# Optimization experiments

Hardware: AMD Instinct MI355X
Metric: run time of the kernel (lower is better)

## Reference

```python
import jax, jax.numpy as jnp
import numpy as np

B, NQ, NV, DIM, HEADS, K = 2, 2048, 2048, 256, 8, 8
HD = DIM // HEADS
HID = 4 * DIM
SCALE = HD ** -0.5
EPS = 1e-5


def setup_inputs() -> dict:
    key = jax.random.key(0)
    ks = jax.random.split(key, 40)
    r = lambda i, s: jax.random.normal(ks[i], s, jnp.float32) * 0.02
    inp = {
        'q': jax.random.normal(ks[0], (B, NQ, DIM), jnp.float32),
        'v': jax.random.normal(ks[1], (B, NV, DIM), jnp.float32),
        'q_pos': jax.random.normal(ks[2], (B, NQ, 3), jnp.float32),
        'v_pos': jax.random.normal(ks[3], (B, NV, 3), jnp.float32),
        'self_knn_index': jax.random.randint(ks[4], (B, NQ, K), 0, NQ, jnp.int32),
        'cross_knn_index': jax.random.randint(ks[5], (B, NQ, K), 0, NV, jnp.int32),
        # LayerNorms (gamma=1, beta=0)
        'norm1_g': jnp.ones(DIM), 'norm1_b': jnp.zeros(DIM),
        'normq_g': jnp.ones(DIM), 'normq_b': jnp.zeros(DIM),
        'normv_g': jnp.ones(DIM), 'normv_b': jnp.zeros(DIM),
        'norm2_g': jnp.ones(DIM), 'norm2_b': jnp.zeros(DIM),
        # self-attention (qkv_bias=False), proj has bias
        'sa_qkv_w': r(6, (DIM, 3 * DIM)),
        'sa_proj_w': r(7, (DIM, DIM)), 'sa_proj_b': jnp.zeros(DIM),
        # cross-attention: q proj and kv proj (no bias), out proj with bias
        'ca_q_w': r(8, (DIM, DIM)),
        'ca_kv_w': r(9, (DIM, 2 * DIM)),
        'ca_proj_w': r(10, (DIM, DIM)), 'ca_proj_b': jnp.zeros(DIM),
        # MLP
        'fc1_w': r(11, (DIM, HID)), 'fc1_b': jnp.zeros(HID),
        'fc2_w': r(12, (HID, DIM)), 'fc2_b': jnp.zeros(DIM),
        # kNN maps
        'knn_w': r(13, (2 * DIM, DIM)), 'knn_b': jnp.zeros(DIM),
        'merge_w': r(14, (2 * DIM, DIM)), 'merge_b': jnp.zeros(DIM),
        'knnx_w': r(15, (2 * DIM, DIM)), 'knnx_b': jnp.zeros(DIM),
        'mergex_w': r(16, (2 * DIM, DIM)), 'mergex_b': jnp.zeros(DIM),
    }
    return inp


def _ln(x, g, b):
    m = x.mean(-1, keepdims=True)
    var = x.var(-1, keepdims=True)
    return (x - m) / jnp.sqrt(var + EPS) * g + b


def _heads(x):  # [B,N,DIM] -> [B,H,N,HD]
    Bx, N, _ = x.shape
    return x.reshape(Bx, N, HEADS, HD).transpose(0, 2, 1, 3)


def _attend(qh, kh, vh, proj_w, proj_b):
    a = jax.nn.softmax(jnp.einsum('bhqd,bhkd->bhqk', qh, kh) * SCALE, axis=-1)
    o = jnp.einsum('bhqk,bhkd->bhqd', a, vh)
    Bx, _, N, _ = o.shape
    o = o.transpose(0, 2, 1, 3).reshape(Bx, N, DIM)
    return o @ proj_w + proj_b


_gather = jax.vmap(lambda pts, idx: pts[idx])  # ([N,D],[Nq,K]) -> [Nq,K,D]


def _knn_feature(qn, vn, idx):  # gather -> diff/cat -> [B,Nq,K,2D]
    local = _gather(vn, idx)                      # [B,Nq,K,D]
    qe = qn[:, :, None, :]                        # [B,Nq,1,D]
    return jnp.concatenate([local - qe, jnp.broadcast_to(qe, local.shape)], -1)


def reference(q, v, q_pos, v_pos, self_knn_index, cross_knn_index,
              norm1_g, norm1_b, normq_g, normq_b, normv_g, normv_b,
              norm2_g, norm2_b, sa_qkv_w, sa_proj_w, sa_proj_b,
              ca_q_w, ca_kv_w, ca_proj_w, ca_proj_b,
              fc1_w, fc1_b, fc2_w, fc2_b,
              knn_w, knn_b, merge_w, merge_b,
              knnx_w, knnx_b, mergex_w, mergex_b):
    # ---- self-attention block with self-kNN branch ----
    nq = _ln(q, norm1_g, norm1_b)
    qkv = nq @ sa_qkv_w
    qh, kh, vh = (_heads(t) for t in jnp.split(qkv, 3, axis=-1))
    sa_out = _attend(qh, kh, vh, sa_proj_w, sa_proj_b)
    f = _knn_feature(nq, nq, self_knn_index)
    knn_out = jax.nn.leaky_relu(f @ knn_w + knn_b, 0.2).max(axis=-2)
    q1 = jnp.concatenate([sa_out, knn_out], -1) @ merge_w + merge_b
    q = q + q1
    # ---- cross-attention block with cross-kNN branch ----
    nq2 = _ln(q, normq_g, normq_b)
    nv = _ln(v, normv_g, normv_b)
    qh = _heads(nq2 @ ca_q_w)
    kh, vh = (_heads(t) for t in jnp.split(nv @ ca_kv_w, 2, axis=-1))
    ca_out = _attend(qh, kh, vh, ca_proj_w, ca_proj_b)
    f = _knn_feature(nq2, nv, cross_knn_index)
    knnx_out = jax.nn.leaky_relu(f @ knnx_w + knnx_b, 0.2).max(axis=-2)
    q2 = jnp.concatenate([ca_out, knnx_out], -1) @ mergex_w + mergex_b
    q = q + q2
    # ---- MLP block ----
    h = _ln(q, norm2_g, norm2_b)
    h = jax.nn.gelu(h @ fc1_w + fc1_b, approximate=False)
    q = q + (h @ fc2_w + fc2_b)
    return q
```

## Files before the change

kernel.cpp:

```cpp
#include <hip/hip_runtime.h>
#include <math.h>

#define NQC   2048
#define NKVC  2048
#define DIMC  256
#define SCALEF 0.2550348810731232f

typedef short bfrag __attribute__((ext_vector_type(8)));
typedef float ffrag __attribute__((ext_vector_type(4)));
typedef unsigned short us8 __attribute__((ext_vector_type(8)));

__device__ __forceinline__ float gelu_exact(float x) {
    return 0.5f * x * (1.0f + erff(x * 0.70710678118654752f));
}
__device__ __forceinline__ unsigned short f2bf(float f) {
    union { float f; unsigned u; } v; v.f = f;
    unsigned r = v.u + 0x7FFFu + ((v.u >> 16) & 1u);
    return (unsigned short)(r >> 16);
}
__device__ __forceinline__ float bf2f(unsigned short u) {
    union { unsigned u; float f; } v; v.u = ((unsigned)u) << 16;
    return v.f;
}
__device__ __forceinline__ float fexp2(float x) {
    float r; asm("v_exp_f32 %0, %1" : "=v"(r) : "v"(x)); return r;
}
__device__ __forceinline__ unsigned cvt_pk_bf16(float lo, float hi) {
    unsigned r; asm("v_cvt_pk_bf16_f32 %0, %1, %2" : "=v"(r) : "v"(lo), "v"(hi));
    return r;
}

__device__ __forceinline__ void ln_row(
    const float* __restrict__ x, const float* __restrict__ g,
    const float* __restrict__ b, unsigned short* __restrict__ y, int row)
{
    int lane = threadIdx.x & 63;
    const float* xr = x + (size_t)row * DIMC + lane * 4;
    float4 vv = *(const float4*)xr;
    float s  = vv.x + vv.y + vv.z + vv.w;
    float sq = vv.x*vv.x + vv.y*vv.y + vv.z*vv.z + vv.w*vv.w;
    #pragma unroll
    for (int off = 32; off >= 1; off >>= 1) {
        s  += __shfl_xor(s, off);
        sq += __shfl_xor(sq, off);
    }
    float mean = s * (1.0f/DIMC);
    float inv  = rsqrtf(sq * (1.0f/DIMC) - mean*mean + 1e-5f);
    float4 gg = *(const float4*)(g + lane*4);
    float4 bb = *(const float4*)(b + lane*4);
    ushort4 o;
    o.x = f2bf((vv.x - mean) * inv * gg.x + bb.x);
    o.y = f2bf((vv.y - mean) * inv * gg.y + bb.y);
    o.z = f2bf((vv.z - mean) * inv * gg.z + bb.z);
    o.w = f2bf((vv.w - mean) * inv * gg.w + bb.w);
    *(ushort4*)(y + (size_t)row * DIMC + lane * 4) = o;
}

__global__ __launch_bounds__(256) void prep_ln(
    const float* __restrict__ qkv, const float* __restrict__ knn,
    const float* __restrict__ proj, const float* __restrict__ merge,
    const float* __restrict__ caq, const float* __restrict__ knnx,
    const float* __restrict__ cakv, const float* __restrict__ projx,
    const float* __restrict__ mergex, const float* __restrict__ fc1,
    const float* __restrict__ fc2, unsigned short* __restrict__ dst,
    const float* __restrict__ lx, const float* __restrict__ lg,
    const float* __restrict__ lb, unsigned short* __restrict__ ly,
    const float* __restrict__ vx, const float* __restrict__ vg,
    const float* __restrict__ vb, unsigned short* __restrict__ vy,
    const float* __restrict__ pb1, const float* __restrict__ mb1, float* __restrict__ bf1o,
    const float* __restrict__ pbx, const float* __restrict__ mbx, float* __restrict__ bfxo)
{
    if (blockIdx.x >= 3584) {
        const float* bp = (blockIdx.x == 3584) ? pb1 : pbx;
        const float* Wm = (blockIdx.x == 3584) ? merge : mergex;
        const float* bm = (blockIdx.x == 3584) ? mb1 : mbx;
        float* o        = (blockIdx.x == 3584) ? bf1o : bfxo;
        int m = threadIdx.x;
        float acc = bm[m];
        for (int k = 0; k < 256; ++k) acc += bp[k] * Wm[(size_t)k * 256 + m];
        o[m] = acc;
        return;
    }
    if (blockIdx.x >= 2560) {
        int row = (blockIdx.x - 2560) * 4 + (threadIdx.x >> 6);
        ln_row(vx, vg, vb, vy, row);
        return;
    }
    if (blockIdx.x >= 1536) {
        int row = (blockIdx.x - 1536) * 4 + (threadIdx.x >> 6);
        ln_row(lx, lg, lb, ly, row);
        return;
    }
    int e = (blockIdx.x * 256 + threadIdx.x) * 4;
    float v[4];
    float scale = 1.0f;
    if (e < 327680) {
        int n = e >> 8, k = e & 255;
        if (n < 768) {
            const float* s = qkv + (size_t)k * 768 + n;
            #pragma unroll
            for (int i = 0; i < 4; ++i) v[i] = s[(size_t)i * 768];
            if (n < 256) scale = SCALEF;
        } else if (n < 1024) {
            const float* s = knn + (size_t)k * 256 + (n - 768);
            #pragma unroll
            for (int i = 0; i < 4; ++i) v[i] = s[(size_t)i * 256];
        } else {
            const float* s = knn + (size_t)k * 256 + (n - 1024);
            #pragma unroll
            for (int i = 0; i < 4; ++i) v[i] = s[65536 + (size_t)i * 256] - s[(size_t)i * 256];
        }
    } else if (e < 393216) {
        int l = e - 327680;
        const float* s = proj + l;
        #pragma unroll
        for (int i = 0; i < 4; ++i) v[i] = s[i];
    } else if (e < 524288) {
        int l = e - 393216, n = l >> 9, k = l & 511;
        const float* s = merge + (size_t)k * 256 + n;
        #pragma unroll
        for (int i = 0; i < 4; ++i) v[i] = s[(size_t)i * 256];
    } else if (e < 655360) {
        int l = e - 524288, n = l >> 8, k = l & 255;
        if (n < 256) {
            const float* s = caq + (size_t)k * 256 + n;
            #pragma unroll
            for (int i = 0; i < 4; ++i) v[i] = s[(size_t)i * 256];
            scale = SCALEF;
        } else {
            const float* s = knnx + (size_t)k * 256 + (n - 256);
            #pragma unroll
            for (int i = 0; i < 4; ++i) v[i] = s[65536 + (size_t)i * 256] - s[(size_t)i * 256];
        }
    } else if (e < 851968) {
        int l = e - 655360, n = l >> 8, k = l & 255;
        if (n < 512) {
            const float* s = cakv + (size_t)k * 512 + n;
            #pragma unroll
            for (int i = 0; i < 4; ++i) v[i] = s[(size_t)i * 512];
        } else {
            const float* s = knnx + (size_t)k * 256 + (n - 512);
            #pragma unroll
            for (int i = 0; i < 4; ++i) v[i] = s[(size_t)i * 256];
        }
    } else if (e < 917504) {
        int l = e - 851968;
        const float* s = projx + l;
        #pragma unroll
        for (int i = 0; i < 4; ++i) v[i] = s[i];
    } else if (e < 1048576) {
        int l = e - 917504, n = l >> 9, k = l & 511;
        const float* s = mergex + (size_t)k * 256 + n;
        #pragma unroll
        for (int i = 0; i < 4; ++i) v[i] = s[(size_t)i * 256];
    } else if (e < 1310720) {
        int l = e - 1048576, n = l >> 8, k = l & 255;
        const float* s = fc1 + (size_t)k * 1024 + n;
        #pragma unroll
        for (int i = 0; i < 4; ++i) v[i] = s[(size_t)i * 1024];
    } else {
        int l = e - 1310720, n = l >> 10, k = l & 1023;
        const float* s = fc2 + (size_t)k * 256 + n;
        #pragma unroll
        for (int i = 0; i < 4; ++i) v[i] = s[(size_t)i * 256];
    }
    ushort4 o;
    o.x = f2bf(v[0] * scale); o.y = f2bf(v[1] * scale);
    o.z = f2bf(v[2] * scale); o.w = f2bf(v[3] * scale);
    *(ushort4*)(dst + e) = o;
}

__global__ __launch_bounds__(256) void ln_b(
    const float* __restrict__ x, const float* __restrict__ g,
    const float* __restrict__ b, unsigned short* __restrict__ y)
{
    ln_row(x, g, b, y, blockIdx.x * 4 + (threadIdx.x >> 6));
}

template<int ACT, int RESID, int OUTBF>
__device__ __forceinline__ void gemm_body(
    const unsigned short* __restrict__ A, int lda,
    const unsigned short* __restrict__ Wt,
    const float* __restrict__ bias,
    const float* __restrict__ resid, int ldr,
    void* __restrict__ Cp, int ldc, int Kc, int row0, int col0,
    unsigned short (* __restrict__ Alds)[72],
    unsigned short (* __restrict__ Wlds)[72])
{
    const int tid = threadIdx.x;
    const int wid = tid >> 6, lane = tid & 63;
    const int lm = lane & 15, quad = lane >> 4;
    const int wr = wid >> 1, wc = wid & 1;
    const int ar = tid >> 2, ac = (tid & 3) * 16;
    const unsigned short* Ag = A  + (size_t)(row0 + ar) * lda + ac;
    const unsigned short* Wg = Wt + (size_t)(col0 + ar) * Kc  + ac;

    us8 a0 = *(const us8*)Ag;
    us8 a1 = *(const us8*)(Ag + 8);
    us8 w0 = *(const us8*)Wg;
    us8 w1 = *(const us8*)(Wg + 8);

    ffrag acc[2][2];
    #pragma unroll
    for (int mi = 0; mi < 2; ++mi)
        #pragma unroll
        for (int ni = 0; ni < 2; ++ni)
            acc[mi][ni] = (ffrag){0.f, 0.f, 0.f, 0.f};

    for (int k0 = 0;;) {
        __syncthreads();
        *(us8*)&Alds[ar][ac]   = a0;
        *(us8*)&Alds[ar][ac+8] = a1;
        *(us8*)&Wlds[ar][ac]   = w0;
        *(us8*)&Wlds[ar][ac+8] = w1;
        __syncthreads();
        k0 += 64;
        if (k0 < Kc) {
            a0 = *(const us8*)(Ag + k0);
            a1 = *(const us8*)(Ag + k0 + 8);
            w0 = *(const us8*)(Wg + k0);
            w1 = *(const us8*)(Wg + k0 + 8);
        }
        #pragma unroll
        for (int kc = 0; kc < 2; ++kc) {
            bfrag af[2], bw[2];
            #pragma unroll
            for (int mi = 0; mi < 2; ++mi)
                af[mi] = *(const bfrag*)&Alds[wr*32 + mi*16 + lm][kc*32 + quad*8];
            #pragma unroll
            for (int ni = 0; ni < 2; ++ni)
                bw[ni] = *(const bfrag*)&Wlds[wc*32 + ni*16 + lm][kc*32 + quad*8];
            #pragma unroll
            for (int mi = 0; mi < 2; ++mi)
                #pragma unroll
                for (int ni = 0; ni < 2; ++ni)
                    acc[mi][ni] = __builtin_amdgcn_mfma_f32_16x16x32_bf16(
                        af[mi], bw[ni], acc[mi][ni], 0, 0, 0);
        }
        if (k0 >= Kc) break;
    }
    #pragma unroll
    for (int mi = 0; mi < 2; ++mi) {
        #pragma unroll
        for (int ni = 0; ni < 2; ++ni) {
            int gr = row0 + wr*32 + mi*16 + quad*4;
            int gc = col0 + wc*32 + ni*16 + lm;
            float bv = bias ? bias[gc] : 0.f;
            #pragma unroll
            for (int r = 0; r < 4; ++r) {
                float o = acc[mi][ni][r] + bv;
                if (ACT == 1) o = gelu_exact(o);
                if (RESID) o += resid[(size_t)(gr + r) * ldr + gc];
                if (OUTBF) ((unsigned short*)Cp)[(size_t)(gr + r) * ldc + gc] = f2bf(o);
                else       ((float*)Cp)[(size_t)(gr + r) * ldc + gc] = o;
            }
        }
    }
}

template<int ACT, int RESID, int OUTBF>
__global__ __launch_bounds__(256) void gemm64(
    const unsigned short* __restrict__ A, int lda,
    const unsigned short* __restrict__ Wt,
    const float* __restrict__ bias,
    const float* __restrict__ resid, int ldr,
    void* __restrict__ Cp, int ldc, int Kc)
{
    __shared__ unsigned short Alds[64][72];
    __shared__ unsigned short Wlds[64][72];
    gemm_body<ACT,RESID,OUTBF>(A, lda, Wt, bias, resid, ldr, Cp, ldc, Kc,
                               blockIdx.y * 64, blockIdx.x * 64, Alds, Wlds);
}

__global__ __launch_bounds__(256) void gemm_qkv_fold(
    const unsigned short* __restrict__ XB, const unsigned short* __restrict__ WT1,
    unsigned short* __restrict__ A1,
    const unsigned short* __restrict__ WTmerge, const unsigned short* __restrict__ projbf,
    unsigned short* __restrict__ WTf1,
    const unsigned short* __restrict__ WTmergex, const unsigned short* __restrict__ projxbf,
    unsigned short* __restrict__ WTfx)
{
    __shared__ unsigned short Alds[64][72];
    __shared__ unsigned short Wlds[64][72];
    const unsigned short *A, *Wt; unsigned short* C;
    int lda, ldc, row0, col0;
    if (blockIdx.y >= 64) {
        if (blockIdx.x >= 16) return;
        row0 = (blockIdx.x >> 2) * 64; col0 = (blockIdx.x & 3) * 64;
        lda = 512; ldc = 256;
        if (blockIdx.y == 64) { A = WTmerge;  Wt = projbf;  C = WTf1; }
        else                  { A = WTmergex; Wt = projxbf; C = WTfx; }
    } else {
        A = XB; Wt = WT1; C = A1; lda = 256; ldc = 1280;
        row0 = blockIdx.y * 64; col0 = blockIdx.x * 64;
    }
    gemm_body<0,0,1>(A, lda, Wt, nullptr, nullptr, 0, C, ldc, 256, row0, col0, Alds, Wlds);
}

template<int ACT, int RESID, int OUTBF>
__global__ __launch_bounds__(512) void gemm64x8(
    const unsigned short* __restrict__ A, int lda,
    const unsigned short* __restrict__ Wt,
    const float* __restrict__ bias,
    const float* __restrict__ resid, int ldr,
    void* __restrict__ Cp, int ldc, int Kc)
{
    __shared__ unsigned short Alds[2][64][72];
    __shared__ unsigned short Wlds[2][64][72];
    __shared__ float Red[64][68];
    const int tid = threadIdx.x;
    const int g = tid >> 8;
    const int t = tid & 255;
    const int wid2 = (tid >> 6) & 3, lane = tid & 63;
    const int lm = lane & 15, quad = lane >> 4;
    const int wr = wid2 >> 1, wc = wid2 & 1;
    const int row0 = blockIdx.y * 64, col0 = blockIdx.x * 64;
    const int ar = t >> 2, ac = (t & 3) * 16;
    const int KH = Kc >> 1;
    const unsigned short* Ag = A  + (size_t)(row0 + ar) * lda + g * KH + ac;
    const unsigned short* Wg = Wt + (size_t)(col0 + ar) * Kc  + g * KH + ac;

    us8 a0 = *(const us8*)Ag;
    us8 a1 = *(const us8*)(Ag + 8);
    us8 w0 = *(const us8*)Wg;
    us8 w1 = *(const us8*)(Wg + 8);

    ffrag acc[2][2];
    #pragma unroll
    for (int mi = 0; mi < 2; ++mi)
        #pragma unroll
        for (int ni = 0; ni < 2; ++ni)
            acc[mi][ni] = (ffrag){0.f, 0.f, 0.f, 0.f};

    for (int k0 = 0;;) {
        __syncthreads();
        *(us8*)&Alds[g][ar][ac]   = a0;
        *(us8*)&Alds[g][ar][ac+8] = a1;
        *(us8*)&Wlds[g][ar][ac]   = w0;
        *(us8*)&Wlds[g][ar][ac+8] = w1;
        __syncthreads();
        k0 += 64;
        if (k0 < KH) {
            a0 = *(const us8*)(Ag + k0);
            a1 = *(const us8*)(Ag + k0 + 8);
            w0 = *(const us8*)(Wg + k0);
            w1 = *(const us8*)(Wg + k0 + 8);
        }
        #pragma unroll
        for (int kc = 0; kc < 2; ++kc) {
            bfrag af[2], bw[2];
            #pragma unroll
            for (int mi = 0; mi < 2; ++mi)
                af[mi] = *(const bfrag*)&Alds[g][wr*32 + mi*16 + lm][kc*32 + quad*8];
            #pragma unroll
            for (int ni = 0; ni < 2; ++ni)
                bw[ni] = *(const bfrag*)&Wlds[g][wc*32 + ni*16 + lm][kc*32 + quad*8];
            #pragma unroll
            for (int mi = 0; mi < 2; ++mi)
                #pragma unroll
                for (int ni = 0; ni < 2; ++ni)
                    acc[mi][ni] = __builtin_amdgcn_mfma_f32_16x16x32_bf16(
                        af[mi], bw[ni], acc[mi][ni], 0, 0, 0);
        }
        if (k0 >= KH) break;
    }
    __syncthreads();
    if (g == 1) {
        #pragma unroll
        for (int mi = 0; mi < 2; ++mi)
            #pragma unroll
            for (int ni = 0; ni < 2; ++ni) {
                int lr = wr*32 + mi*16 + quad*4;
                int lc = wc*32 + ni*16 + lm;
                #pragma unroll
                for (int r = 0; r < 4; ++r)
                    Red[lr + r][lc] = acc[mi][ni][r];
            }
    }
    __syncthreads();
    if (g == 0) {
        #pragma unroll
        for (int mi = 0; mi < 2; ++mi) {
            #pragma unroll
            for (int ni = 0; ni < 2; ++ni) {
                int lr = wr*32 + mi*16 + quad*4;
                int lc = wc*32 + ni*16 + lm;
                int gr = row0 + lr;
                int gc = col0 + lc;
                float bv = bias ? bias[gc] : 0.f;
                #pragma unroll
                for (int r = 0; r < 4; ++r) {
                    float o = acc[mi][ni][r] + Red[lr + r][lc] + bv;
                    if (ACT == 1) o = gelu_exact(o);
                    if (RESID) o += resid[(size_t)(gr + r) * ldr + gc];
                    if (OUTBF) ((unsigned short*)Cp)[(size_t)(gr + r) * ldc + gc] = f2bf(o);
                    else       ((float*)Cp)[(size_t)(gr + r) * ldc + gc] = o;
                }
            }
        }
    }
}

__global__ __launch_bounds__(512) void gemm64x8f(
    const unsigned short* __restrict__ Op, const float* __restrict__ Lp,
    const unsigned short* __restrict__ Akn,
    const unsigned short* __restrict__ Wat,
    const unsigned short* __restrict__ Wkn,
    const float* __restrict__ bias,
    const float* __restrict__ resid,
    float* __restrict__ Cp)
{
    __shared__ unsigned short Alds[2][64][72];
    __shared__ unsigned short Wlds[2][64][72];
    __shared__ float Red[64][68];
    const int tid = threadIdx.x;
    const int g = tid >> 8;
    const int t = tid & 255;
    const int wid2 = (tid >> 6) & 3, lane = tid & 63;
    const int lm = lane & 15, quad = lane >> 4;
    const int wr = wid2 >> 1, wc = wid2 & 1;
    const int row0 = blockIdx.y * 64, col0 = blockIdx.x * 64;
    const int ar = t >> 2, ac = (t & 3) * 16;
    const int grow = row0 + ar;

    const unsigned short* O0 = Op + (size_t)grow * 256 + ac;
    const unsigned short* O1 = Op + (size_t)(4096 + grow) * 256 + ac;
    const float* L0 = Lp + (size_t)grow * 8;
    const float* L1 = Lp + (size_t)(4096 + grow) * 8;
    const unsigned short* Ak = Akn + (size_t)grow * 512 + ac;
    const unsigned short* Wg = g ? Wkn + (size_t)(col0 + ar) * 512 + ac
                                 : Wat + (size_t)(col0 + ar) * 256 + ac;

    us8 a0, a1, o10, o11;
    float li = 0.f;
    if (g == 0) {
        a0  = *(const us8*)O0;  a1  = *(const us8*)(O0 + 8);
        o10 = *(const us8*)O1;  o11 = *(const us8*)(O1 + 8);
        li  = 1.0f / (L0[ac >> 5] + L1[ac >> 5]);
    } else {
        a0 = *(const us8*)Ak;   a1 = *(const us8*)(Ak + 8);
    }
    us8 w0 = *(const us8*)Wg;
    us8 w1 = *(const us8*)(Wg + 8);

    ffrag acc[2][2];
    #pragma unroll
    for (int mi = 0; mi < 2; ++mi)
        #pragma unroll
        for (int ni = 0; ni < 2; ++ni)
            acc[mi][ni] = (ffrag){0.f, 0.f, 0.f, 0.f};

    for (int k0 = 0;;) {
        us8 s0 = a0, s1 = a1;
        if (g == 0) {
            #pragma unroll
            for (int i = 0; i < 8; ++i) {
                s0[i] = f2bf((bf2f(a0[i]) + bf2f(o10[i])) * li);
                s1[i] = f2bf((bf2f(a1[i]) + bf2f(o11[i])) * li);
            }
        }
        __syncthreads();
        *(us8*)&Alds[g][ar][ac]   = s0;
        *(us8*)&Alds[g][ar][ac+8] = s1;
        *(us8*)&Wlds[g][ar][ac]   = w0;
        *(us8*)&Wlds[g][ar][ac+8] = w1;
        __syncthreads();
        k0 += 64;
        if (k0 < 256) {
            if (g == 0) {
                a0  = *(const us8*)(O0 + k0);  a1  = *(const us8*)(O0 + k0 + 8);
                o10 = *(const us8*)(O1 + k0);  o11 = *(const us8*)(O1 + k0 + 8);
                li  = 1.0f / (L0[(k0 + ac) >> 5] + L1[(k0 + ac) >> 5]);
            } else {
                a0 = *(const us8*)(Ak + k0);   a1 = *(const us8*)(Ak + k0 + 8);
            }
            w0 = *(const us8*)(Wg + k0);
            w1 = *(const us8*)(Wg + k0 + 8);
        }
        #pragma unroll
        for (int kc = 0; kc < 2; ++kc) {
            bfrag af[2], bw[2];
            #pragma unroll
            for (int mi = 0; mi < 2; ++mi)
                af[mi] = *(const bfrag*)&Alds[g][wr*32 + mi*16 + lm][kc*32 + quad*8];
            #pragma unroll
            for (int ni = 0; ni < 2; ++ni)
                bw[ni] = *(const bfrag*)&Wlds[g][wc*32 + ni*16 + lm][kc*32 + quad*8];
            #pragma unroll
            for (int mi = 0; mi < 2; ++mi)
                #pragma unroll
                for (int ni = 0; ni < 2; ++ni)
                    acc[mi][ni] = __builtin_amdgcn_mfma_f32_16x16x32_bf16(
                        af[mi], bw[ni], acc[mi][ni], 0, 0, 0);
        }
        if (k0 >= 256) break;
    }
    __syncthreads();
    if (g == 1) {
        #pragma unroll
        for (int mi = 0; mi < 2; ++mi)
            #pragma unroll
            for (int ni = 0; ni < 2; ++ni) {
                int lr = wr*32 + mi*16 + quad*4;
                int lc = wc*32 + ni*16 + lm;
                #pragma unroll
                for (int r = 0; r < 4; ++r)
                    Red[lr + r][lc] = acc[mi][ni][r];
            }
    }
    __syncthreads();
    if (g == 0) {
        #pragma unroll
        for (int mi = 0; mi < 2; ++mi) {
            #pragma unroll
            for (int ni = 0; ni < 2; ++ni) {
                int lr = wr*32 + mi*16 + quad*4;
                int lc = wc*32 + ni*16 + lm;
                int gr = row0 + lr;
                int gc = col0 + lc;
                float bv = bias[gc];
                #pragma unroll
                for (int r = 0; r < 4; ++r)
                    Cp[(size_t)(gr + r) * 256 + gc] =
                        acc[mi][ni][r] + Red[lr + r][lc] + bv
                        + resid[(size_t)(gr + r) * 256 + gc];
            }
        }
    }
}

__global__ __launch_bounds__(256) void gemm64_dual(
    const unsigned short* __restrict__ XB,
    const unsigned short* __restrict__ NVB,
    const unsigned short* __restrict__ WT2,
    const unsigned short* __restrict__ WT3,
    unsigned short* __restrict__ A2,
    unsigned short* __restrict__ A3)
{
    __shared__ unsigned short Alds[64][72];
    __shared__ unsigned short Wlds[64][72];
    const unsigned short* A; const unsigned short* Wt;
    unsigned short* C; int ldc, col0;
    if (blockIdx.x < 8) { A = XB;  Wt = WT2; C = A2; ldc = 512; col0 = blockIdx.x * 64; }
    else                { A = NVB; Wt = WT3; C = A3; ldc = 768; col0 = (blockIdx.x - 8) * 64; }
    gemm_body<0,0,1>(A, 256, Wt, nullptr, nullptr, 0, C, ldc, 256,
                     blockIdx.y * 64, col0, Alds, Wlds);
}

__global__ __launch_bounds__(256) void attn_gather(
    const unsigned short* __restrict__ Qp, int ldq,
    const unsigned short* __restrict__ Kp, int ldk,
    const unsigned short* __restrict__ Vp, int ldv,
    unsigned short* __restrict__ Op, float* __restrict__ Lp,
    const unsigned short* __restrict__ P, int ldp,
    const unsigned short* __restrict__ Base, int ldb,
    const float* __restrict__ gbias, const int* __restrict__ idx,
    unsigned short* __restrict__ gout, int ldgo)
{
    __shared__ unsigned short Klds[64][40];
    __shared__ __align__(16) unsigned short Vt[32][72];
    __shared__ __align__(16) unsigned short Plds[4][16][72];
    int tid = threadIdx.x, wid = tid >> 6, lane = tid & 63;

    if (blockIdx.z >= 4) {
        int gbid = blockIdx.x + 32 * (blockIdx.y + 8 * (blockIdx.z - 4));
        int q = gbid * 4 + wid;
        int b = q >> 11;
        int c = lane * 4;
        ushort4 bu = *(const ushort4*)(Base + (size_t)q * ldb + c);
        float4 bi = *(const float4*)(gbias + c);
        float bsx = bf2f(bu.x) + bi.x, bsy = bf2f(bu.y) + bi.y;
        float bsz = bf2f(bu.z) + bi.z, bsw = bf2f(bu.w) + bi.w;
        float4 acc = make_float4(-3e38f, -3e38f, -3e38f, -3e38f);
        const int* ip = idx + (size_t)q * 8;
        #pragma unroll
        for (int k = 0; k < 8; ++k) {
            int j = ip[k];
            ushort4 pu = *(const ushort4*)(P + ((size_t)(b * NKVC + j)) * ldp + c);
            float t;
            t = bsx + bf2f(pu.x); t = t > 0.f ? t : 0.2f * t; acc.x = fmaxf(acc.x, t);
            t = bsy + bf2f(pu.y); t = t > 0.f ? t : 0.2f * t; acc.y = fmaxf(acc.y, t);
            t = bsz + bf2f(pu.z); t = t > 0.f ? t : 0.2f * t; acc.z = fmaxf(acc.z, t);
            t = bsw + bf2f(pu.w); t = t > 0.f ? t : 0.2f * t; acc.w = fmaxf(acc.w, t);
        }
        ushort4 o;
        o.x = f2bf(acc.x); o.y = f2bf(acc.y); o.z = f2bf(acc.z); o.w = f2bf(acc.w);
        *(ushort4*)(gout + (size_t)q * ldgo + c) = o;
        return;
    }

    int zc = blockIdx.z, bb = zc >> 1, ck = zc & 1;
    int h = blockIdx.y;
    int hoff = h * 32;
    int lm = lane & 15, quad = lane >> 4;
    size_t qbase  = (size_t)bb * NQC;
    size_t kvbase = (size_t)bb * NKVC;
    int q0 = blockIdx.x * 64 + wid * 16;

    bfrag aq = *(const bfrag*)(Qp + (qbase + q0 + lm) * (size_t)ldq + hoff + quad * 8);

    float l_r[4] = {0.f, 0.f, 0.f, 0.f};
    ffrag oacc[2];
    oacc[0] = (ffrag){0.f, 0.f, 0.f, 0.f};
    oacc[1] = (ffrag){0.f, 0.f, 0.f, 0.f};

    const int kkey = tid >> 2, kd0 = (tid & 3) * 8;
    const int vkey = tid & 63, vd0 = (tid >> 6) * 8;
    const int vcol = ((vkey & 15) << 2) | (vkey >> 4);
    const unsigned short* kg0 = Kp + (kvbase + kkey) * (size_t)ldk + hoff + kd0;
    const unsigned short* vg0 = Vp + (kvbase + vkey) * (size_t)ldv + hoff + vd0;

    for (int kt = ck * 16; kt < ck * 16 + 16; ++kt) {
        us8 kv = *(const us8*)(kg0 + (size_t)kt * 64 * ldk);
        us8 vv = *(const us8*)(vg0 + (size_t)kt * 64 * ldv);
        __syncthreads();
        *(us8*)&Klds[kkey][kd0] = kv;
        #pragma unroll
        for (int i = 0; i < 8; ++i) Vt[vd0 + i][vcol] = vv[i];
        __syncthreads();

        ffrag sacc[4];
        #pragma unroll
        for (int t = 0; t < 4; ++t) {
            bfrag bk = *(const bfrag*)&Klds[t*16 + lm][quad * 8];
            sacc[t] = __builtin_amdgcn_mfma_f32_16x16x32_bf16(
                aq, bk, (ffrag){0.f,0.f,0.f,0.f}, 0, 0, 0);
        }

        #pragma unroll
        for (int r = 0; r < 4; ++r) {
            float p0 = fexp2(sacc[0][r]), p1 = fexp2(sacc[1][r]);
            float p2 = fexp2(sacc[2][r]), p3 = fexp2(sacc[3][r]);
            l_r[r] += (p0 + p1) + (p2 + p3);
            unsigned u0 = cvt_pk_bf16(p0, p1);
            unsigned u1 = cvt_pk_bf16(p2, p3);
            *(uint2*)&Plds[wid][quad*4 + r][lm << 2] = make_uint2(u0, u1);
        }
        asm volatile("s_waitcnt lgkmcnt(0)" ::: "memory");

        #pragma unroll
        for (int kc = 0; kc < 2; ++kc) {
            bfrag ap = *(const bfrag*)&Plds[wid][lm][kc*32 + quad*8];
            #pragma unroll
            for (int nt = 0; nt < 2; ++nt) {
                bfrag bv = *(const bfrag*)&Vt[nt*16 + lm][kc*32 + quad*8];
                oacc[nt] = __builtin_amdgcn_mfma_f32_16x16x32_bf16(
                    ap, bv, oacc[nt], 0, 0, 0);
            }
        }
    }
    #pragma unroll
    for (int nt = 0; nt < 2; ++nt)
        #pragma unroll
        for (int r = 0; r < 4; ++r)
            Op[((size_t)ck * 4096 + qbase + q0 + quad*4 + r) * 256 + hoff + nt*16 + lm]
                = f2bf(oacc[nt][r]);
    #pragma unroll
    for (int r = 0; r < 4; ++r) {
        float l = l_r[r];
        l += __shfl_xor(l, 1);
        l += __shfl_xor(l, 2);
        l += __shfl_xor(l, 4);
        l += __shfl_xor(l, 8);
        if (lm == 0)
            Lp[((size_t)ck * 4096 + qbase + q0 + quad*4 + r) * 8 + h] = l;
    }
}

extern "C" void kernel_launch(void* const* d_in, const int* in_sizes, int n_in,
                              void* d_out, int out_size, void* d_ws, size_t ws_size,
                              hipStream_t stream) {
    const float* q_in   = (const float*)d_in[0];
    const float* v_in   = (const float*)d_in[1];
    const int*   idx_s  = (const int*)d_in[4];
    const int*   idx_x  = (const int*)d_in[5];
    const float* n1g = (const float*)d_in[6],  *n1b = (const float*)d_in[7];
    const float* nqg = (const float*)d_in[8],  *nqb = (const float*)d_in[9];
    const float* nvg = (const float*)d_in[10], *nvb = (const float*)d_in[11];
    const float* n2g = (const float*)d_in[12], *n2b = (const float*)d_in[13];
    const float* sa_qkv_w  = (const float*)d_in[14];
    const float* sa_proj_w = (const float*)d_in[15];
    const float* sa_proj_b = (const float*)d_in[16];
    const float* ca_q_w    = (const float*)d_in[17];
    const float* ca_kv_w   = (const float*)d_in[18];
    const float* ca_proj_w = (const float*)d_in[19];
    const float* ca_proj_b = (const float*)d_in[20];
    const float* fc1_w = (const float*)d_in[21], *fc1_b = (const float*)d_in[22];
    const float* fc2_w = (const float*)d_in[23], *fc2_b = (const float*)d_in[24];
    const float* knn_w   = (const float*)d_in[25], *knn_b   = (const float*)d_in[26];
    const float* merge_w = (const float*)d_in[27], *merge_b = (const float*)d_in[28];
    const float* knnx_w  = (const float*)d_in[29], *knnx_b  = (const float*)d_in[30];
    const float* mergex_w = (const float*)d_in[31], *mergex_b = (const float*)d_in[32];
    float* out = (float*)d_out;

    unsigned short* A1      = (unsigned short*)d_ws;
    unsigned short* A2      = A1;
    unsigned short* A3      = A1 + (size_t)4096 * 512;
    unsigned short* Hb      = A1;
    unsigned short* KN      = A1 + (size_t)4096 * 1280;
    unsigned short* CC      = KN;
    unsigned short* XB      = CC + (size_t)4096 * 512;
    unsigned short* NVB     = XB + (size_t)4096 * 256;
    unsigned short* WT      = NVB + (size_t)4096 * 256;
    unsigned short* WT1     = WT;
    unsigned short* projbf  = WT + 327680;
    unsigned short* WTmerge = WT + 393216;
    unsigned short* WT2     = WT + 524288;
    unsigned short* WT3     = WT + 655360;
    unsigned short* projxbf = WT + 851968;
    unsigned short* WTmergex= WT + 917504;
    unsigned short* WTfc1   = WT + 1048576;
    unsigned short* WTfc2   = WT + 1310720;
    unsigned short* Opart   = WT + 1572864;
    float* Lpart = (float*)(Opart + (size_t)2 * 4096 * 256);
    unsigned short* WTf1 = (unsigned short*)(Lpart + (size_t)2 * 4096 * 8);
    unsigned short* WTfx = WTf1 + 65536;
    float* bf1 = (float*)(WTfx + 65536);
    float* bfx = bf1 + 256;

    dim3 blk(256), blk8(512);
    dim3 gAG(NQC / 64, 8, 8);

    prep_ln<<<dim3(3586), blk, 0, stream>>>(sa_qkv_w, knn_w, sa_proj_w, merge_w,
        ca_q_w, knnx_w, ca_kv_w, ca_proj_w, mergex_w, fc1_w, fc2_w, WT,
        q_in, n1g, n1b, XB,
        v_in, nvg, nvb, NVB,
        sa_proj_b, merge_b, bf1,
        ca_proj_b, mergex_b, bfx);

    gemm_qkv_fold<<<dim3(20,66), blk, 0, stream>>>(XB, WT1, A1,
        WTmerge, projbf, WTf1, WTmergex, projxbf, WTfx);
    attn_gather<<<gAG, blk, 0, stream>>>(A1, 1280, A1+256, 1280, A1+512, 1280,
        Opart, Lpart, A1+768, 1280, A1+1024, 1280, knn_b, idx_s, CC+256, 512);
    gemm64x8f<<<dim3(4,64), blk8, 0, stream>>>(Opart, Lpart, CC+256,
        WTf1, WTmerge+256, bf1, q_in, out);

    ln_b<<<dim3(1024), blk, 0, stream>>>(out, nqg, nqb, XB);
    gemm64_dual<<<dim3(20,64), blk, 0, stream>>>(XB, NVB, WT2, WT3, A2, A3);
    attn_gather<<<gAG, blk, 0, stream>>>(A2, 512, A3, 768, A3+256, 768,
        Opart, Lpart, A3+512, 768, A2+256, 512, knnx_b, idx_x, CC+256, 512);
    gemm64x8f<<<dim3(4,64), blk8, 0, stream>>>(Opart, Lpart, CC+256,
        WTfx, WTmergex+256, bfx, out, out);

    ln_b<<<dim3(1024), blk, 0, stream>>>(out, n2g, n2b, XB);
    gemm64<1,0,1><<<dim3(16,64), blk, 0, stream>>>(XB, 256, WTfc1,
        fc1_b, nullptr, 0, Hb, 1024, 256);
    gemm64x8<0,1,0><<<dim3(4,64), blk8, 0, stream>>>(Hb, 1024, WTfc2,
        fc2_b, out, 256, out, 256, 1024);
}
```

Before: 245.3 us.

## Write V pre-transposed from projection GEMMs and drop split-K attention partials

```diff
diff --git a/kernel.cpp b/kernel.cpp
--- a/kernel.cpp
+++ b/kernel.cpp
@@ -177,7 +177,7 @@
     ln_row(x, g, b, y, blockIdx.x * 4 + (threadIdx.x >> 6));
 }
 
-template<int ACT, int RESID, int OUTBF>
+template<int ACT, int RESID, int OUTBF, int VTM>
 __device__ __forceinline__ void gemm_body(
     const unsigned short* __restrict__ A, int lda,
     const unsigned short* __restrict__ Wt,
@@ -185,7 +185,8 @@
     const float* __restrict__ resid, int ldr,
     void* __restrict__ Cp, int ldc, int Kc, int row0, int col0,
     unsigned short (* __restrict__ Alds)[72],
-    unsigned short (* __restrict__ Wlds)[72])
+    unsigned short (* __restrict__ Wlds)[72],
+    unsigned short* __restrict__ vt, int vlo)
 {
     const int tid = threadIdx.x;
     const int wid = tid >> 6, lane = tid & 63;
@@ -245,14 +246,27 @@
         for (int ni = 0; ni < 2; ++ni) {
             int gr = row0 + wr*32 + mi*16 + quad*4;
             int gc = col0 + wc*32 + ni*16 + lm;
-            float bv = bias ? bias[gc] : 0.f;
-            #pragma unroll
-            for (int r = 0; r < 4; ++r) {
-                float o = acc[mi][ni][r] + bv;
-                if (ACT == 1) o = gelu_exact(o);
-                if (RESID) o += resid[(size_t)(gr + r) * ldr + gc];
-                if (OUTBF) ((unsigned short*)Cp)[(size_t)(gr + r) * ldc + gc] = f2bf(o);
-                else       ((float*)Cp)[(size_t)(gr + r) * ldc + gc] = o;
+            if (VTM && gc >= vlo && gc < vlo + 256) {
+                int cv = gc - vlo, hh = cv >> 5, dd = cv & 31;
+                int b = gr >> 11;
+                int kin = gr & 63;
+                int kblk = (gr & 2047) >> 6;
+                int pos = ((kin & 15) << 2) | (kin >> 4);
+                unsigned short* vp = vt + (((size_t)(b*8+hh)*32 + dd) * 2048)
+                                       + kblk * 64 + pos;
+                #pragma unroll
+                for (int r = 0; r < 4; ++r)
+                    vp[r * 4] = f2bf(acc[mi][ni][r]);
+            } else {
+                float bv = bias ? bias[gc] : 0.f;
+                #pragma unroll
+                for (int r = 0; r < 4; ++r) {
+                    float o = acc[mi][ni][r] + bv;
+                    if (ACT == 1) o = gelu_exact(o);
+                    if (RESID) o += resid[(size_t)(gr + r) * ldr + gc];
+                    if (OUTBF) ((unsigned short*)Cp)[(size_t)(gr + r) * ldc + gc] = f2bf(o);
+                    else       ((float*)Cp)[(size_t)(gr + r) * ldc + gc] = o;
+                }
             }
         }
     }
@@ -268,8 +282,9 @@
 {
     __shared__ unsigned short Alds[64][72];
     __shared__ unsigned short Wlds[64][72];
-    gemm_body<ACT,RESID,OUTBF>(A, lda, Wt, bias, resid, ldr, Cp, ldc, Kc,
-                               blockIdx.y * 64, blockIdx.x * 64, Alds, Wlds);
+    gemm_body<ACT,RESID,OUTBF,0>(A, lda, Wt, bias, resid, ldr, Cp, ldc, Kc,
+                                 blockIdx.y * 64, blockIdx.x * 64, Alds, Wlds,
+                                 nullptr, 0);
 }
 
 __global__ __launch_bounds__(256) void gemm_qkv_fold(
@@ -278,23 +293,25 @@
     const unsigned short* __restrict__ WTmerge, const unsigned short* __restrict__ projbf,
     unsigned short* __restrict__ WTf1,
     const unsigned short* __restrict__ WTmergex, const unsigned short* __restrict__ projxbf,
-    unsigned short* __restrict__ WTfx)
+    unsigned short* __restrict__ WTfx,
+    unsigned short* __restrict__ VT)
 {
     __shared__ unsigned short Alds[64][72];
     __shared__ unsigned short Wlds[64][72];
     const unsigned short *A, *Wt; unsigned short* C;
-    int lda, ldc, row0, col0;
+    int lda, ldc, row0, col0, vlo;
     if (blockIdx.y >= 64) {
         if (blockIdx.x >= 16) return;
         row0 = (blockIdx.x >> 2) * 64; col0 = (blockIdx.x & 3) * 64;
-        lda = 512; ldc = 256;
+        lda = 512; ldc = 256; vlo = 1 << 30;
         if (blockIdx.y == 64) { A = WTmerge;  Wt = projbf;  C = WTf1; }
         else                  { A = WTmergex; Wt = projxbf; C = WTfx; }
     } else {
-        A = XB; Wt = WT1; C = A1; lda = 256; ldc = 1280;
+        A = XB; Wt = WT1; C = A1; lda = 256; ldc = 1280; vlo = 512;
         row0 = blockIdx.y * 64; col0 = blockIdx.x * 64;
     }
-    gemm_body<0,0,1>(A, lda, Wt, nullptr, nullptr, 0, C, ldc, 256, row0, col0, Alds, Wlds);
+    gemm_body<0,0,1,1>(A, lda, Wt, nullptr, nullptr, 0, C, ldc, 256, row0, col0,
+                       Alds, Wlds, VT, vlo);
 }
 
 template<int ACT, int RESID, int OUTBF>
@@ -402,10 +419,10 @@
 }
 
 __global__ __launch_bounds__(512) void gemm64x8f(
-    const unsigned short* __restrict__ Op, const float* __restrict__ Lp,
+    const unsigned short* __restrict__ O,
     const unsigned short* __restrict__ Akn,
-    const unsigned short* __restrict__ Wat,
-    const unsigned short* __restrict__ Wkn,
+    const unsigned short* __restrict__ W0,
+    const unsigned short* __restrict__ W1,
     const float* __restrict__ bias,
     const float* __restrict__ resid,
     float* __restrict__ Cp)
@@ -423,23 +440,13 @@
     const int ar = t >> 2, ac = (t & 3) * 16;
     const int grow = row0 + ar;
 
-    const unsigned short* O0 = Op + (size_t)grow * 256 + ac;
-    const unsigned short* O1 = Op + (size_t)(4096 + grow) * 256 + ac;
-    const float* L0 = Lp + (size_t)grow * 8;
-    const float* L1 = Lp + (size_t)(4096 + grow) * 8;
-    const unsigned short* Ak = Akn + (size_t)grow * 512 + ac;
-    const unsigned short* Wg = g ? Wkn + (size_t)(col0 + ar) * 512 + ac
-                                 : Wat + (size_t)(col0 + ar) * 256 + ac;
-
-    us8 a0, a1, o10, o11;
-    float li = 0.f;
-    if (g == 0) {
-        a0  = *(const us8*)O0;  a1  = *(const us8*)(O0 + 8);
-        o10 = *(const us8*)O1;  o11 = *(const us8*)(O1 + 8);
-        li  = 1.0f / (L0[ac >> 5] + L1[ac >> 5]);
-    } else {
-        a0 = *(const us8*)Ak;   a1 = *(const us8*)(Ak + 8);
-    }
+    const unsigned short* Ag = g ? Akn + (size_t)grow * 512 + ac
+                                 : O   + (size_t)grow * 256 + ac;
+    const unsigned short* Wg = g ? W1 + (size_t)(col0 + ar) * 512 + ac
+                                 : W0 + (size_t)(col0 + ar) * 256 + ac;
+
+    us8 a0 = *(const us8*)Ag;
+    us8 a1 = *(const us8*)(Ag + 8);
     us8 w0 = *(const us8*)Wg;
     us8 w1 = *(const us8*)(Wg + 8);
 
@@ -451,29 +458,16 @@
             acc[mi][ni] = (ffrag){0.f, 0.f, 0.f, 0.f};
 
     for (int k0 = 0;;) {
-        us8 s0 = a0, s1 = a1;
-        if (g == 0) {
-            #pragma unroll
-            for (int i = 0; i < 8; ++i) {
-                s0[i] = f2bf((bf2f(a0[i]) + bf2f(o10[i])) * li);
-                s1[i] = f2bf((bf2f(a1[i]) + bf2f(o11[i])) * li);
-            }
-        }
         __syncthreads();
-        *(us8*)&Alds[g][ar][ac]   = s0;
-        *(us8*)&Alds[g][ar][ac+8] = s1;
+        *(us8*)&Alds[g][ar][ac]   = a0;
+        *(us8*)&Alds[g][ar][ac+8] = a1;
         *(us8*)&Wlds[g][ar][ac]   = w0;
         *(us8*)&Wlds[g][ar][ac+8] = w1;
         __syncthreads();
         k0 += 64;
         if (k0 < 256) {
-            if (g == 0) {
-                a0  = *(const us8*)(O0 + k0);  a1  = *(const us8*)(O0 + k0 + 8);
-                o10 = *(const us8*)(O1 + k0);  o11 = *(const us8*)(O1 + k0 + 8);
-                li  = 1.0f / (L0[(k0 + ac) >> 5] + L1[(k0 + ac) >> 5]);
-            } else {
-                a0 = *(const us8*)(Ak + k0);   a1 = *(const us8*)(Ak + k0 + 8);
-            }
+            a0 = *(const us8*)(Ag + k0);
+            a1 = *(const us8*)(Ag + k0 + 8);
             w0 = *(const us8*)(Wg + k0);
             w1 = *(const us8*)(Wg + k0 + 8);
         }
@@ -535,23 +529,24 @@
     const unsigned short* __restrict__ WT2,
     const unsigned short* __restrict__ WT3,
     unsigned short* __restrict__ A2,
-    unsigned short* __restrict__ A3)
+    unsigned short* __restrict__ A3,
+    unsigned short* __restrict__ VT)
 {
     __shared__ unsigned short Alds[64][72];
     __shared__ unsigned short Wlds[64][72];
     const unsigned short* A; const unsigned short* Wt;
-    unsigned short* C; int ldc, col0;
-    if (blockIdx.x < 8) { A = XB;  Wt = WT2; C = A2; ldc = 512; col0 = blockIdx.x * 64; }
-    else                { A = NVB; Wt = WT3; C = A3; ldc = 768; col0 = (blockIdx.x - 8) * 64; }
-    gemm_body<0,0,1>(A, 256, Wt, nullptr, nullptr, 0, C, ldc, 256,
-                     blockIdx.y * 64, col0, Alds, Wlds);
+    unsigned short* C; int ldc, col0, vlo;
+    if (blockIdx.x < 8) { A = XB;  Wt = WT2; C = A2; ldc = 512; col0 = blockIdx.x * 64; vlo = 1 << 30; }
+    else                { A = NVB; Wt = WT3; C = A3; ldc = 768; col0 = (blockIdx.x - 8) * 64; vlo = 256; }
+    gemm_body<0,0,1,1>(A, 256, Wt, nullptr, nullptr, 0, C, ldc, 256,
+                       blockIdx.y * 64, col0, Alds, Wlds, VT, vlo);
 }
 
 __global__ __launch_bounds__(256) void attn_gather(
     const unsigned short* __restrict__ Qp, int ldq,
     const unsigned short* __restrict__ Kp, int ldk,
-    const unsigned short* __restrict__ Vp, int ldv,
-    unsigned short* __restrict__ Op, float* __restrict__ Lp,
+    const unsigned short* __restrict__ VT,
+    unsigned short* __restrict__ Op,
     const unsigned short* __restrict__ P, int ldp,
     const unsigned short* __restrict__ Base, int ldb,
     const float* __restrict__ gbias, const int* __restrict__ idx,
@@ -559,11 +554,11 @@
 {
     __shared__ unsigned short Klds[64][40];
     __shared__ __align__(16) unsigned short Vt[32][72];
-    __shared__ __align__(16) unsigned short Plds[4][16][72];
+    __shared__ __align__(16) unsigned short Plds[4][2][16][72];
     int tid = threadIdx.x, wid = tid >> 6, lane = tid & 63;
 
-    if (blockIdx.z >= 4) {
-        int gbid = blockIdx.x + 32 * (blockIdx.y + 8 * (blockIdx.z - 4));
+    if (blockIdx.z >= 1) {
+        int gbid = blockIdx.x + 32 * (blockIdx.y + 8 * (blockIdx.z - 1));
         int q = gbid * 4 + wid;
         int b = q >> 11;
         int c = lane * 4;
@@ -589,82 +584,94 @@
         return;
     }
 
-    int zc = blockIdx.z, bb = zc >> 1, ck = zc & 1;
+    int bb = blockIdx.x >> 4, qc = blockIdx.x & 15;
     int h = blockIdx.y;
     int hoff = h * 32;
     int lm = lane & 15, quad = lane >> 4;
     size_t qbase  = (size_t)bb * NQC;
     size_t kvbase = (size_t)bb * NKVC;
-    int q0 = blockIdx.x * 64 + wid * 16;
-
-    bfrag aq = *(const bfrag*)(Qp + (qbase + q0 + lm) * (size_t)ldq + hoff + quad * 8);
-
-    float l_r[4] = {0.f, 0.f, 0.f, 0.f};
-    ffrag oacc[2];
-    oacc[0] = (ffrag){0.f, 0.f, 0.f, 0.f};
-    oacc[1] = (ffrag){0.f, 0.f, 0.f, 0.f};
+    int q0 = qc * 128 + wid * 32;
+
+    bfrag aq0 = *(const bfrag*)(Qp + (qbase + q0 + lm)      * (size_t)ldq + hoff + quad * 8);
+    bfrag aq1 = *(const bfrag*)(Qp + (qbase + q0 + 16 + lm) * (size_t)ldq + hoff + quad * 8);
+
+    float l0[4] = {0.f, 0.f, 0.f, 0.f};
+    float l1[4] = {0.f, 0.f, 0.f, 0.f};
+    ffrag oacc[2][2];
+    #pragma unroll
+    for (int i = 0; i < 2; ++i)
+        #pragma unroll
+        for (int j = 0; j < 2; ++j)
+            oacc[i][j] = (ffrag){0.f, 0.f, 0.f, 0.f};
 
     const int kkey = tid >> 2, kd0 = (tid & 3) * 8;
-    const int vkey = tid & 63, vd0 = (tid >> 6) * 8;
-    const int vcol = ((vkey & 15) << 2) | (vkey >> 4);
+    const int vrow = tid >> 3, vp0 = (tid & 7) * 8;
     const unsigned short* kg0 = Kp + (kvbase + kkey) * (size_t)ldk + hoff + kd0;
-    const unsigned short* vg0 = Vp + (kvbase + vkey) * (size_t)ldv + hoff + vd0;
-
-    for (int kt = ck * 16; kt < ck * 16 + 16; ++kt) {
+    const unsigned short* vg0 = VT + (((size_t)bb * 8 + h) * 32 + vrow) * 2048 + vp0;
+
+    for (int kt = 0; kt < 32; ++kt) {
         us8 kv = *(const us8*)(kg0 + (size_t)kt * 64 * ldk);
-        us8 vv = *(const us8*)(vg0 + (size_t)kt * 64 * ldv);
+        us8 vv = *(const us8*)(vg0 + kt * 64);
         __syncthreads();
         *(us8*)&Klds[kkey][kd0] = kv;
-        #pragma unroll
-        for (int i = 0; i < 8; ++i) Vt[vd0 + i][vcol] = vv[i];
+        *(us8*)&Vt[vrow][vp0]   = vv;
         __syncthreads();
 
-        ffrag sacc[4];
+        ffrag s0[4], s1[4];
         #pragma unroll
         for (int t = 0; t < 4; ++t) {
             bfrag bk = *(const bfrag*)&Klds[t*16 + lm][quad * 8];
-            sacc[t] = __builtin_amdgcn_mfma_f32_16x16x32_bf16(
-                aq, bk, (ffrag){0.f,0.f,0.f,0.f}, 0, 0, 0);
+            s0[t] = __builtin_amdgcn_mfma_f32_16x16x32_bf16(
+                aq0, bk, (ffrag){0.f,0.f,0.f,0.f}, 0, 0, 0);
+            s1[t] = __builtin_amdgcn_mfma_f32_16x16x32_bf16(
+                aq1, bk, (ffrag){0.f,0.f,0.f,0.f}, 0, 0, 0);
         }
 
         #pragma unroll
         for (int r = 0; r < 4; ++r) {
-            float p0 = fexp2(sacc[0][r]), p1 = fexp2(sacc[1][r]);
-            float p2 = fexp2(sacc[2][r]), p3 = fexp2(sacc[3][r]);
-            l_r[r] += (p0 + p1) + (p2 + p3);
-            unsigned u0 = cvt_pk_bf16(p0, p1);
-            unsigned u1 = cvt_pk_bf16(p2, p3);
-            *(uint2*)&Plds[wid][quad*4 + r][lm << 2] = make_uint2(u0, u1);
+            float p0 = fexp2(s0[0][r]), p1 = fexp2(s0[1][r]);
+            float p2 = fexp2(s0[2][r]), p3 = fexp2(s0[3][r]);
+            l0[r] += (p0 + p1) + (p2 + p3);
+            *(uint2*)&Plds[wid][0][quad*4 + r][lm << 2] =
+                make_uint2(cvt_pk_bf16(p0, p1), cvt_pk_bf16(p2, p3));
+            float u0 = fexp2(s1[0][r]), u1 = fexp2(s1[1][r]);
+            float u2 = fexp2(s1[2][r]), u3 = fexp2(s1[3][r]);
+            l1[r] += (u0 + u1) + (u2 + u3);
+            *(uint2*)&Plds[wid][1][quad*4 + r][lm << 2] =
+                make_uint2(cvt_pk_bf16(u0, u1), cvt_pk_bf16(u2, u3));
         }
         asm volatile("s_waitcnt lgkmcnt(0)" ::: "memory");
 
         #pragma unroll
         for (int kc = 0; kc < 2; ++kc) {
-            bfrag ap = *(const bfrag*)&Plds[wid][lm][kc*32 + quad*8];
-            #pragma unroll
-            for (int nt = 0; nt < 2; ++nt) {
-                bfrag bv = *(const bfrag*)&Vt[nt*16 + lm][kc*32 + quad*8];
-                oacc[nt] = __builtin_amdgcn_mfma_f32_16x16x32_bf16(
-                    ap, bv, oacc[nt], 0, 0, 0);
-            }
-        }
+            bfrag bv0 = *(const bfrag*)&Vt[lm][kc*32 + quad*8];
+            bfrag bv1 = *(const bfrag*)&Vt[16 + lm][kc*32 + quad*8];
+            bfrag ap0 = *(const bfrag*)&Plds[wid][0][lm][kc*32 + quad*8];
+            bfrag ap1 = *(const bfrag*)&Plds[wid][1][lm][kc*32 + quad*8];
+            oacc[0][0] = __builtin_amdgcn_mfma_f32_16x16x32_bf16(ap0, bv0, oacc[0][0], 0, 0, 0);
+            oacc[0][1] = __builtin_amdgcn_mfma_f32_16x16x32_bf16(ap0, bv1, oacc[0][1], 0, 0, 0);
+            oacc[1][0] = __builtin_amdgcn_mfma_f32_16x16x32_bf16(ap1, bv0, oacc[1][0], 0, 0, 0);
+            oacc[1][1] = __builtin_amdgcn_mfma_f32_16x16x32_bf16(ap1, bv1, oacc[1][1], 0, 0, 0);
+        }
+    }
+    #pragma unroll
+    for (int r = 0; r < 4; ++r) {
+        float a = l0[r], b = l1[r];
+        a += __shfl_xor(a, 1); a += __shfl_xor(a, 2);
+        a += __shfl_xor(a, 4); a += __shfl_xor(a, 8);
+        b += __shfl_xor(b, 1); b += __shfl_xor(b, 2);
+        b += __shfl_xor(b, 4); b += __shfl_xor(b, 8);
+        l0[r] = 1.0f / a; l1[r] = 1.0f / b;
     }
     #pragma unroll
     for (int nt = 0; nt < 2; ++nt)
         #pragma unroll
-        for (int r = 0; r < 4; ++r)
-            Op[((size_t)ck * 4096 + qbase + q0 + quad*4 + r) * 256 + hoff + nt*16 + lm]
-                = f2bf(oacc[nt][r]);
-    #pragma unroll
-    for (int r = 0; r < 4; ++r) {
-        float l = l_r[r];
-        l += __shfl_xor(l, 1);
-        l += __shfl_xor(l, 2);
-        l += __shfl_xor(l, 4);
-        l += __shfl_xor(l, 8);
-        if (lm == 0)
-            Lp[((size_t)ck * 4096 + qbase + q0 + quad*4 + r) * 8 + h] = l;
-    }
+        for (int r = 0; r < 4; ++r) {
+            Op[(qbase + q0 + quad*4 + r) * 256 + hoff + nt*16 + lm]
+                = f2bf(oacc[0][nt][r] * l0[r]);
+            Op[(qbase + q0 + 16 + quad*4 + r) * 256 + hoff + nt*16 + lm]
+                = f2bf(oacc[1][nt][r] * l1[r]);
+        }
 }
 
 extern "C" void kernel_launch(void* const* d_in, const int* in_sizes, int n_in,
@@ -712,14 +719,14 @@
     unsigned short* WTfc1   = WT + 1048576;
     unsigned short* WTfc2   = WT + 1310720;
     unsigned short* Opart   = WT + 1572864;
-    float* Lpart = (float*)(Opart + (size_t)2 * 4096 * 256);
-    unsigned short* WTf1 = (unsigned short*)(Lpart + (size_t)2 * 4096 * 8);
-    unsigned short* WTfx = WTf1 + 65536;
+    unsigned short* WTf1    = Opart + (size_t)4096 * 256;
+    unsigned short* WTfx    = WTf1 + 65536;
     float* bf1 = (float*)(WTfx + 65536);
     float* bfx = bf1 + 256;
+    unsigned short* VT = (unsigned short*)(bfx + 256);
 
     dim3 blk(256), blk8(512);
-    dim3 gAG(NQC / 64, 8, 8);
+    dim3 gAG(32, 8, 5);
 
     prep_ln<<<dim3(3586), blk, 0, stream>>>(sa_qkv_w, knn_w, sa_proj_w, merge_w,
         ca_q_w, knnx_w, ca_kv_w, ca_proj_w, mergex_w, fc1_w, fc2_w, WT,
@@ -729,17 +736,17 @@
         ca_proj_b, mergex_b, bfx);
 
     gemm_qkv_fold<<<dim3(20,66), blk, 0, stream>>>(XB, WT1, A1,
-        WTmerge, projbf, WTf1, WTmergex, projxbf, WTfx);
-    attn_gather<<<gAG, blk, 0, stream>>>(A1, 1280, A1+256, 1280, A1+512, 1280,
-        Opart, Lpart, A1+768, 1280, A1+1024, 1280, knn_b, idx_s, CC+256, 512);
-    gemm64x8f<<<dim3(4,64), blk8, 0, stream>>>(Opart, Lpart, CC+256,
+        WTmerge, projbf, WTf1, WTmergex, projxbf, WTfx, VT);
+    attn_gather<<<gAG, blk, 0, stream>>>(A1, 1280, A1+256, 1280, VT,
+        Opart, A1+768, 1280, A1+1024, 1280, knn_b, idx_s, CC+256, 512);
+    gemm64x8f<<<dim3(4,64), blk8, 0, stream>>>(Opart, CC+256,
         WTf1, WTmerge+256, bf1, q_in, out);
 
     ln_b<<<dim3(1024), blk, 0, stream>>>(out, nqg, nqb, XB);
-    gemm64_dual<<<dim3(20,64), blk, 0, stream>>>(XB, NVB, WT2, WT3, A2, A3);
-    attn_gather<<<gAG, blk, 0, stream>>>(A2, 512, A3, 768, A3+256, 768,
-        Opart, Lpart, A3+512, 768, A2+256, 512, knnx_b, idx_x, CC+256, 512);
-    gemm64x8f<<<dim3(4,64), blk8, 0, stream>>>(Opart, Lpart, CC+256,
+    gemm64_dual<<<dim3(20,64), blk, 0, stream>>>(XB, NVB, WT2, WT3, A2, A3, VT);
+    attn_gather<<<gAG, blk, 0, stream>>>(A2, 512, A3, 768, VT,
+        Opart, A3+512, 768, A2+256, 512, knnx_b, idx_x, CC+256, 512);
+    gemm64x8f<<<dim3(4,64), blk8, 0, stream>>>(Opart, CC+256,
         WTfx, WTmergex+256, bfx, out, out);
 
     ln_b<<<dim3(1024), blk, 0, stream>>>(out, n2g, n2b, XB);
```

Measured after the change: 263.6 us. +7.5%, slower.
